# Kernel optimization log

Measured on AMD Instinct MI355X. Metric: run time of the kernel, lower is better.

The kernel has to match this reference:

```python
import jax, jax.numpy as jnp
import numpy as np

EMB_DIM = 1024
NUM_HEADS = 16
HEAD_DIM = EMB_DIM // NUM_HEADS


def setup_inputs() -> dict:
    key = jax.random.key(0)
    ks = jax.random.split(key, 6)
    B, T, D = 4, 2048, EMB_DIM
    s = 1.0 / np.sqrt(D)
    return {
        "x": jax.random.normal(ks[0], (B, T, D), dtype=jnp.float32),
        "Wq": jax.random.normal(ks[1], (D, D), dtype=jnp.float32) * s,
        "Wk": jax.random.normal(ks[2], (D, D), dtype=jnp.float32) * s,
        "Wv": jax.random.normal(ks[3], (D, D), dtype=jnp.float32) * s,
        "Wo": jax.random.normal(ks[4], (D, D), dtype=jnp.float32) * s,
        "bo": jax.random.normal(ks[5], (D,), dtype=jnp.float32) * 0.01,
    }


def reference(x, Wq, Wk, Wv, Wo, bo):
    B, T, D = x.shape
    H, Hd = NUM_HEADS, HEAD_DIM
    # Linear projections (torch Linear: x @ W.T); weights here stored as [in, out]
    q = (x @ Wq).reshape(B, T, H, Hd).transpose(0, 2, 1, 3)  # [B,H,T,Hd]
    k = (x @ Wk).reshape(B, T, H, Hd).transpose(0, 2, 1, 3)
    v = (x @ Wv).reshape(B, T, H, Hd).transpose(0, 2, 1, 3)
    scores = jnp.einsum("bhqd,bhkd->bhqk", q, k) / jnp.sqrt(jnp.float32(Hd))
    causal = jnp.tril(jnp.ones((T, T), dtype=bool))
    scores = jnp.where(causal, scores, -jnp.inf)
    weights = jax.nn.softmax(scores, axis=-1)  # drop_rate=0 -> dropout is identity
    ctx = jnp.einsum("bhqk,bhkd->bhqd", weights, v)
    ctx = ctx.transpose(0, 2, 1, 3).reshape(B, T, D)
    return ctx @ Wo + bo
```

## Files before the change

kernel.cpp:

```cpp
#include <hip/hip_runtime.h>
#include <hip/hip_bf16.h>
#include <math.h>

#define TSEQ   2048
#define BATCH  4
#define DIM    1024
#define NH     16
#define HD     64
#define MTOT   (BATCH*TSEQ)
#define LDQKV  (3*DIM)

typedef __attribute__((ext_vector_type(8))) short bf16x8;
typedef __attribute__((ext_vector_type(4))) float f32x4;

__device__ __forceinline__ unsigned short f2bf(float f) {
    unsigned int b = __float_as_uint(f);
    b = (b + 0x7fffu + ((b >> 16) & 1u)) >> 16;
    return (unsigned short)b;
}

__device__ __forceinline__ unsigned cvt_pk_bf16(float lo, float hi) {
    unsigned r;
    asm("v_cvt_pk_bf16_f32 %0, %1, %2" : "=v"(r) : "v"(lo), "v"(hi));
    return r;
}

__device__ __forceinline__ void glds16(const void* g, void* l) {
    __builtin_amdgcn_global_load_lds(
        (const __attribute__((address_space(1))) void*)g,
        (__attribute__((address_space(3))) void*)l, 16, 0, 0);
}

__global__ __launch_bounds__(256)
void cvt_x(const float* __restrict__ in, unsigned short* __restrict__ out, int n8)
{
    int i = blockIdx.x * 256 + threadIdx.x;
    if (i >= n8) return;
    const float4* p = (const float4*)in + 2 * (size_t)i;
    float4 a = p[0], b = p[1];
    bf16x8 o;
    o[0] = (short)f2bf(a.x); o[1] = (short)f2bf(a.y);
    o[2] = (short)f2bf(a.z); o[3] = (short)f2bf(a.w);
    o[4] = (short)f2bf(b.x); o[5] = (short)f2bf(b.y);
    o[6] = (short)f2bf(b.z); o[7] = (short)f2bf(b.w);
    *((bf16x8*)out + i) = o;
}

__global__ __launch_bounds__(256)
void cvt_tr(const float* __restrict__ W, unsigned short* __restrict__ WT)
{
    __shared__ float t[32][33];
    const int x = threadIdx.x, y0 = threadIdx.y;
    const int bx = blockIdx.x, by = blockIdx.y;
#pragma unroll
    for (int j = 0; j < 4; ++j)
        t[y0 + j*8][x] = W[(size_t)(by*32 + y0 + j*8) * DIM + bx*32 + x];
    __syncthreads();
#pragma unroll
    for (int j = 0; j < 4; ++j)
        WT[(size_t)(bx*32 + y0 + j*8) * DIM + by*32 + x] = f2bf(t[x][y0 + j*8]);
}

template<bool F32OUT>
__global__ __launch_bounds__(256)
void gemm_glds(const unsigned short* __restrict__ A, const unsigned short* __restrict__ BT,
               const float* __restrict__ bias, void* __restrict__ Cout,
               const int M, const int N, const int K)
{
    __shared__ unsigned short As[128*32];
    __shared__ unsigned short Bs[128*32];
    const int t = threadIdx.x;
    const int w = t >> 6, lane = t & 63, g = lane >> 4, li = lane & 15;
    const int wm = (w >> 1) * 64, wn = (w & 1) * 64;
    const int m0 = blockIdx.x * 128, n0 = blockIdx.y * 128;

    f32x4 acc[4][4] = {};

    const int r_a  = w*32 + (lane >> 2);
    const int r_b  = r_a + 16;
    const int slot = lane & 3;
    const int sc0  = slot ^ ((r_a >> 1) & 3);
    const int sc1  = slot ^ ((r_b >> 1) & 3);

    const unsigned short* Ap0 = &A [(size_t)(m0 + r_a) * K + sc0*8];
    const unsigned short* Ap1 = &A [(size_t)(m0 + r_b) * K + sc1*8];
    const unsigned short* Bp0 = &BT[(size_t)(n0 + r_a) * K + sc0*8];
    const unsigned short* Bp1 = &BT[(size_t)(n0 + r_b) * K + sc1*8];
    unsigned short* AsW0 = &As[w*1024];
    unsigned short* AsW1 = &As[w*1024 + 512];
    unsigned short* BsW0 = &Bs[w*1024];
    unsigned short* BsW1 = &Bs[w*1024 + 512];

    char* AsB = (char*)As;
    char* BsB = (char*)Bs;

    for (int kt = 0; kt < K; kt += 32) {
        __syncthreads();
        glds16(Ap0 + kt, AsW0);
        glds16(Ap1 + kt, AsW1);
        glds16(Bp0 + kt, BsW0);
        glds16(Bp1 + kt, BsW1);
        __syncthreads();

        bf16x8 af[4], bfv[4];
#pragma unroll
        for (int mi = 0; mi < 4; ++mi) {
            const int r = wm + mi*16 + li;
            af[mi] = *(const bf16x8*)(AsB + r*64 + ((g ^ ((r >> 1) & 3)) * 16));
        }
#pragma unroll
        for (int ni = 0; ni < 4; ++ni) {
            const int r = wn + ni*16 + li;
            bfv[ni] = *(const bf16x8*)(BsB + r*64 + ((g ^ ((r >> 1) & 3)) * 16));
        }
#pragma unroll
        for (int mi = 0; mi < 4; ++mi)
#pragma unroll
            for (int ni = 0; ni < 4; ++ni)
                acc[mi][ni] = __builtin_amdgcn_mfma_f32_16x16x32_bf16(
                    af[mi], bfv[ni], acc[mi][ni], 0, 0, 0);
    }

#pragma unroll
    for (int mi = 0; mi < 4; ++mi)
#pragma unroll
        for (int ni = 0; ni < 4; ++ni) {
            const int gr = m0 + wm + mi*16 + 4*g;
            const int gc = n0 + wn + ni*16 + li;
#pragma unroll
            for (int r = 0; r < 4; ++r) {
                const float v = acc[mi][ni][r];
                if (F32OUT)
                    ((float*)Cout)[(size_t)(gr + r) * N + gc] = v + bias[gc];
                else
                    ((unsigned short*)Cout)[(size_t)(gr + r) * N + gc] = f2bf(v);
            }
        }
}

#define SCL2E 0.18033688f

__global__ __launch_bounds__(256)
void attn_bf16(const unsigned short* __restrict__ QKV, unsigned short* __restrict__ O)
{
    __shared__ unsigned short Ks[64*64];
    __shared__ unsigned short VT[64*64];
    const int t = threadIdx.x;
    const int w = t >> 6, lane = t & 63, g = lane >> 4, li = lane & 15;
    const int qt = (int)gridDim.x - 1 - (int)blockIdx.x;
    const int bh = blockIdx.y, b = bh >> 4, h = bh & 15;
    const int q0 = qt * 64;
    const size_t rowbase = (size_t)b * TSEQ;
    const int cq = h*HD, ck = DIM + h*HD, cv = 2*DIM + h*HD;

    bf16x8 qa[2];
#pragma unroll
    for (int ks = 0; ks < 2; ++ks)
        qa[ks] = *(const bf16x8*)&QKV[(rowbase + q0 + w*16 + li) * LDQKV + cq + 8*g + 32*ks];

    f32x4 ctx[4] = {};
    float m_i = -INFINITY, l_i = 0.f;

    char* KsB = (char*)Ks;
    char* VTB = (char*)VT;

    const int krow = lane >> 3;
    const int kch0 = (lane & 7) ^ (krow & 3);
    const int kch1 = kch0 ^ 4;
    const int kr0 = 16*w + krow, kr1 = kr0 + 8;
    const int dc0 = 2*w, dc1 = 2*w + 1;

    for (int kv = 0; kv <= qt; ++kv) {
        const size_t nb = rowbase + (size_t)kv * 64;
        bf16x8 v0 = *(const bf16x8*)&QKV[(nb + lane) * LDQKV + cv + dc0*8];
        bf16x8 v1 = *(const bf16x8*)&QKV[(nb + lane) * LDQKV + cv + dc1*8];
        __syncthreads();
        glds16(&QKV[(nb + kr0) * LDQKV + ck + kch0*8], &Ks[(2*w    )*512]);
        glds16(&QKV[(nb + kr1) * LDQKV + ck + kch1*8], &Ks[(2*w + 1)*512]);
#pragma unroll
        for (int j = 0; j < 8; ++j) {
            const int d0 = dc0*8 + j, d1 = dc1*8 + j;
            *(unsigned short*)(VTB + d0*128 + (((lane >> 3) ^ ((d0 & 3) | ((d0 & 8) >> 1))) * 16) + (lane & 7)*2) = (unsigned short)v0[j];
            *(unsigned short*)(VTB + d1*128 + (((lane >> 3) ^ ((d1 & 3) | ((d1 & 8) >> 1))) * 16) + (lane & 7)*2) = (unsigned short)v1[j];
        }
        __syncthreads();

        f32x4 s[4] = {};
#pragma unroll
        for (int nt = 0; nt < 4; ++nt) {
            const int r  = 32*(nt >> 1) + 4*(nt & 1) + 8*(li >> 2) + (li & 3);
            const int sz = (r & 3) | ((r & 8) >> 1);
#pragma unroll
            for (int ks = 0; ks < 2; ++ks) {
                bf16x8 kb = *(const bf16x8*)(KsB + r*128 + (((g + 4*ks) ^ sz) * 16));
                s[nt] = __builtin_amdgcn_mfma_f32_16x16x32_bf16(kb, qa[ks], s[nt], 0, 0, 0);
            }
        }
        if (kv == qt) {
#pragma unroll
            for (int nt = 0; nt < 4; ++nt) {
                const int kb0 = 32*(nt >> 1) + 4*(nt & 1) + 8*g;
#pragma unroll
                for (int reg = 0; reg < 4; ++reg)
                    if (kb0 + reg > w*16 + li) s[nt][reg] = -INFINITY;
            }
        }

        float mx = s[0][0];
#pragma unroll
        for (int nt = 0; nt < 4; ++nt)
#pragma unroll
            for (int reg = 0; reg < 4; ++reg) mx = fmaxf(mx, s[nt][reg]);
        mx = fmaxf(mx, __shfl_xor(mx, 16));
        mx = fmaxf(mx, __shfl_xor(mx, 32));
        mx *= SCL2E;
        if (mx > m_i + 8.f) {
            const float sc = exp2f(m_i - mx);
            m_i = mx;
            l_i *= sc;
#pragma unroll
            for (int n2 = 0; n2 < 4; ++n2) ctx[n2] *= sc;
        }
        float rs = 0.f;
#pragma unroll
        for (int nt = 0; nt < 4; ++nt)
#pragma unroll
            for (int reg = 0; reg < 4; ++reg) {
                const float p = exp2f(fmaf(s[nt][reg], SCL2E, -m_i));
                s[nt][reg] = p;
                rs += p;
            }
        rs += __shfl_xor(rs, 16);
        rs += __shfl_xor(rs, 32);
        l_i += rs;

        unsigned pk[4][2];
#pragma unroll
        for (int nt = 0; nt < 4; ++nt) {
            pk[nt][0] = cvt_pk_bf16(s[nt][0], s[nt][1]);
            pk[nt][1] = cvt_pk_bf16(s[nt][2], s[nt][3]);
        }

#pragma unroll
        for (int ks2 = 0; ks2 < 2; ++ks2) {
            union { unsigned u[4]; bf16x8 v; } pf;
            pf.u[0] = pk[2*ks2][0]; pf.u[1] = pk[2*ks2][1];
            pf.u[2] = pk[2*ks2+1][0]; pf.u[3] = pk[2*ks2+1][1];
#pragma unroll
            for (int n2 = 0; n2 < 4; ++n2) {
                const int r  = n2*16 + li;
                const int sz = (li & 3) | ((li & 8) >> 1);
                bf16x8 vb = *(const bf16x8*)(VTB + r*128 + (((g + 4*ks2) ^ sz) * 16));
                ctx[n2] = __builtin_amdgcn_mfma_f32_16x16x32_bf16(vb, pf.v, ctx[n2], 0, 0, 0);
            }
        }
    }

    const float inv = 1.f / l_i;
    const size_t row = rowbase + q0 + w*16 + li;
    unsigned* Ou = (unsigned*)O;
#pragma unroll
    for (int n2 = 0; n2 < 4; ++n2) {
        const size_t base = (row * DIM + h*HD + n2*16 + 4*g) >> 1;
        Ou[base    ] = cvt_pk_bf16(ctx[n2][0]*inv, ctx[n2][1]*inv);
        Ou[base + 1] = cvt_pk_bf16(ctx[n2][2]*inv, ctx[n2][3]*inv);
    }
}

extern "C" void kernel_launch(void* const* d_in, const int* in_sizes, int n_in,
                              void* d_out, int out_size, void* d_ws, size_t ws_size,
                              hipStream_t stream)
{
    const float* x  = (const float*)d_in[0];
    const float* Wq = (const float*)d_in[1];
    const float* Wk = (const float*)d_in[2];
    const float* Wv = (const float*)d_in[3];
    const float* Wo = (const float*)d_in[4];
    const float* bo = (const float*)d_in[5];
    float* out = (float*)d_out;

    char* ws = (char*)d_ws;
    unsigned short* xb    = (unsigned short*)(ws);
    unsigned short* qkv   = (unsigned short*)(ws + (16u << 20));
    unsigned short* ctb   = (unsigned short*)(ws + (64u << 20));
    unsigned short* WTall = (unsigned short*)(ws + (80u << 20));
    unsigned short* WoT   = (unsigned short*)(ws + (86u << 20));

    cvt_x<<<MTOT*DIM/8/256, 256, 0, stream>>>(x, xb, MTOT*DIM/8);
    dim3 tb(32, 8), tg(32, 32);
    cvt_tr<<<tg, tb, 0, stream>>>(Wq, WTall);
    cvt_tr<<<tg, tb, 0, stream>>>(Wk, WTall + (size_t)DIM*DIM);
    cvt_tr<<<tg, tb, 0, stream>>>(Wv, WTall + (size_t)2*DIM*DIM);
    cvt_tr<<<tg, tb, 0, stream>>>(Wo, WoT);

    gemm_glds<false><<<dim3(MTOT/128, LDQKV/128), 256, 0, stream>>>(
        xb, WTall, nullptr, qkv, MTOT, LDQKV, DIM);

    attn_bf16<<<dim3(TSEQ/64, BATCH*NH), 256, 0, stream>>>(qkv, ctb);

    gemm_glds<true><<<dim3(MTOT/128, DIM/128), 256, 0, stream>>>(
        ctb, WoT, bo, out, MTOT, DIM, DIM);
}
```

Baseline: 363.7 us.

## Double-buffer LDS tiles in GEMM and attention kernels to overlap loads

Both the projection GEMM and the attention kernel now keep two LDS buffers and issue the global-to-LDS loads for the next K/V or k-tile before computing on the current one. This drops one barrier per iteration and lets memory latency hide behind MFMA work. The cost is doubled shared memory per block, which may reduce occupancy, and more live registers for the prefetched V data in attention.

```diff
diff --git a/kernel.cpp b/kernel.cpp
--- a/kernel.cpp
+++ b/kernel.cpp
@@ -67,8 +67,8 @@
                const float* __restrict__ bias, void* __restrict__ Cout,
                const int M, const int N, const int K)
 {
-    __shared__ unsigned short As[128*32];
-    __shared__ unsigned short Bs[128*32];
+    __shared__ unsigned short As[2][128*32];
+    __shared__ unsigned short Bs[2][128*32];
     const int t = threadIdx.x;
     const int w = t >> 6, lane = t & 63, g = lane >> 4, li = lane & 15;
     const int wm = (w >> 1) * 64, wn = (w & 1) * 64;
@@ -86,22 +86,24 @@
     const unsigned short* Ap1 = &A [(size_t)(m0 + r_b) * K + sc1*8];
     const unsigned short* Bp0 = &BT[(size_t)(n0 + r_a) * K + sc0*8];
     const unsigned short* Bp1 = &BT[(size_t)(n0 + r_b) * K + sc1*8];
-    unsigned short* AsW0 = &As[w*1024];
-    unsigned short* AsW1 = &As[w*1024 + 512];
-    unsigned short* BsW0 = &Bs[w*1024];
-    unsigned short* BsW1 = &Bs[w*1024 + 512];
-
-    char* AsB = (char*)As;
-    char* BsB = (char*)Bs;
-
+
+    glds16(Ap0, &As[0][w*1024]);
+    glds16(Ap1, &As[0][w*1024 + 512]);
+    glds16(Bp0, &Bs[0][w*1024]);
+    glds16(Bp1, &Bs[0][w*1024 + 512]);
+    __syncthreads();
+
+    int cur = 0;
     for (int kt = 0; kt < K; kt += 32) {
-        __syncthreads();
-        glds16(Ap0 + kt, AsW0);
-        glds16(Ap1 + kt, AsW1);
-        glds16(Bp0 + kt, BsW0);
-        glds16(Bp1 + kt, BsW1);
-        __syncthreads();
-
+        if (kt + 32 < K) {
+            glds16(Ap0 + kt + 32, &As[cur^1][w*1024]);
+            glds16(Ap1 + kt + 32, &As[cur^1][w*1024 + 512]);
+            glds16(Bp0 + kt + 32, &Bs[cur^1][w*1024]);
+            glds16(Bp1 + kt + 32, &Bs[cur^1][w*1024 + 512]);
+        }
+
+        char* AsB = (char*)&As[cur][0];
+        char* BsB = (char*)&Bs[cur][0];
         bf16x8 af[4], bfv[4];
 #pragma unroll
         for (int mi = 0; mi < 4; ++mi) {
@@ -119,6 +121,11 @@
             for (int ni = 0; ni < 4; ++ni)
                 acc[mi][ni] = __builtin_amdgcn_mfma_f32_16x16x32_bf16(
                     af[mi], bfv[ni], acc[mi][ni], 0, 0, 0);
+
+        if (kt + 32 < K) {
+            __syncthreads();
+            cur ^= 1;
+        }
     }
 
 #pragma unroll
@@ -143,8 +150,8 @@
 __global__ __launch_bounds__(256)
 void attn_bf16(const unsigned short* __restrict__ QKV, unsigned short* __restrict__ O)
 {
-    __shared__ unsigned short Ks[64*64];
-    __shared__ unsigned short VT[64*64];
+    __shared__ unsigned short Ks[2][64*64];
+    __shared__ unsigned short VT[2][64*64];
     const int t = threadIdx.x;
     const int w = t >> 6, lane = t & 63, g = lane >> 4, li = lane & 15;
     const int qt = (int)gridDim.x - 1 - (int)blockIdx.x;
@@ -161,29 +168,41 @@
     f32x4 ctx[4] = {};
     float m_i = -INFINITY, l_i = 0.f;
 
-    char* KsB = (char*)Ks;
-    char* VTB = (char*)VT;
-
     const int krow = lane >> 3;
     const int kch0 = (lane & 7) ^ (krow & 3);
     const int kch1 = kch0 ^ 4;
     const int kr0 = 16*w + krow, kr1 = kr0 + 8;
     const int dc0 = 2*w, dc1 = 2*w + 1;
 
-    for (int kv = 0; kv <= qt; ++kv) {
-        const size_t nb = rowbase + (size_t)kv * 64;
+    {
+        const size_t nb = rowbase;
+        glds16(&QKV[(nb + kr0) * LDQKV + ck + kch0*8], &Ks[0][(2*w    )*512]);
+        glds16(&QKV[(nb + kr1) * LDQKV + ck + kch1*8], &Ks[0][(2*w + 1)*512]);
         bf16x8 v0 = *(const bf16x8*)&QKV[(nb + lane) * LDQKV + cv + dc0*8];
         bf16x8 v1 = *(const bf16x8*)&QKV[(nb + lane) * LDQKV + cv + dc1*8];
-        __syncthreads();
-        glds16(&QKV[(nb + kr0) * LDQKV + ck + kch0*8], &Ks[(2*w    )*512]);
-        glds16(&QKV[(nb + kr1) * LDQKV + ck + kch1*8], &Ks[(2*w + 1)*512]);
+        char* VTB = (char*)&VT[0][0];
 #pragma unroll
         for (int j = 0; j < 8; ++j) {
             const int d0 = dc0*8 + j, d1 = dc1*8 + j;
             *(unsigned short*)(VTB + d0*128 + (((lane >> 3) ^ ((d0 & 3) | ((d0 & 8) >> 1))) * 16) + (lane & 7)*2) = (unsigned short)v0[j];
             *(unsigned short*)(VTB + d1*128 + (((lane >> 3) ^ ((d1 & 3) | ((d1 & 8) >> 1))) * 16) + (lane & 7)*2) = (unsigned short)v1[j];
         }
-        __syncthreads();
+    }
+    __syncthreads();
+
+    int cur = 0;
+    for (int kv = 0; kv <= qt; ++kv) {
+        bf16x8 vn0, vn1;
+        if (kv < qt) {
+            const size_t nb = rowbase + (size_t)(kv + 1) * 64;
+            glds16(&QKV[(nb + kr0) * LDQKV + ck + kch0*8], &Ks[cur^1][(2*w    )*512]);
+            glds16(&QKV[(nb + kr1) * LDQKV + ck + kch1*8], &Ks[cur^1][(2*w + 1)*512]);
+            vn0 = *(const bf16x8*)&QKV[(nb + lane) * LDQKV + cv + dc0*8];
+            vn1 = *(const bf16x8*)&QKV[(nb + lane) * LDQKV + cv + dc1*8];
+        }
+
+        char* KsB = (char*)&Ks[cur][0];
+        char* VTB = (char*)&VT[cur][0];
 
         f32x4 s[4] = {};
 #pragma unroll
@@ -241,6 +260,16 @@
             pk[nt][1] = cvt_pk_bf16(s[nt][2], s[nt][3]);
         }
 
+        if (kv < qt) {
+            char* VTN = (char*)&VT[cur^1][0];
+#pragma unroll
+            for (int j = 0; j < 8; ++j) {
+                const int d0 = dc0*8 + j, d1 = dc1*8 + j;
+                *(unsigned short*)(VTN + d0*128 + (((lane >> 3) ^ ((d0 & 3) | ((d0 & 8) >> 1))) * 16) + (lane & 7)*2) = (unsigned short)vn0[j];
+                *(unsigned short*)(VTN + d1*128 + (((lane >> 3) ^ ((d1 & 3) | ((d1 & 8) >> 1))) * 16) + (lane & 7)*2) = (unsigned short)vn1[j];
+            }
+        }
+
 #pragma unroll
         for (int ks2 = 0; ks2 < 2; ++ks2) {
             union { unsigned u[4]; bf16x8 v; } pf;
@@ -253,6 +282,11 @@
                 bf16x8 vb = *(const bf16x8*)(VTB + r*128 + (((g + 4*ks2) ^ sz) * 16));
                 ctx[n2] = __builtin_amdgcn_mfma_f32_16x16x32_bf16(vb, pf.v, ctx[n2], 0, 0, 0);
             }
+        }
+
+        if (kv < qt) {
+            __syncthreads();
+            cur ^= 1;
         }
     }
 
```

After: 379.2 us. 1.04x slower.
